# Kernel optimization log

Measured on AMD Instinct MI355X. Metric: run time of the kernel, lower is better.

The kernel has to match this reference:

```python
import jax, jax.numpy as jnp
import numpy as np

B, T, K, H = 256, 2048, 64, 256
NUM_PRED = 512


def setup_inputs() -> dict:
    key = jax.random.key(0)
    ks = jax.random.split(key, 13)
    s = 0.05
    G = 4 * H
    return {
        "input": jax.random.normal(ks[0], (B, T), jnp.float32),
        "conv_w": jax.random.normal(ks[1], (K,), jnp.float32) * s,
        "conv_b": jax.random.normal(ks[2], (K,), jnp.float32) * s,
        "W_ih0": jax.random.normal(ks[3], (G, K), jnp.float32) * s,
        "W_hh0": jax.random.normal(ks[4], (G, H), jnp.float32) * s,
        "b_ih0": jax.random.normal(ks[5], (G,), jnp.float32) * s,
        "b_hh0": jax.random.normal(ks[6], (G,), jnp.float32) * s,
        "W_ih1": jax.random.normal(ks[7], (G, H), jnp.float32) * s,
        "W_hh1": jax.random.normal(ks[8], (G, H), jnp.float32) * s,
        "b_ih1": jax.random.normal(ks[9], (G,), jnp.float32) * s,
        "b_hh1": jax.random.normal(ks[10], (G,), jnp.float32) * s,
        "lin_w": jax.random.normal(ks[11], (1, H), jnp.float32) * s,
        "lin_b": jax.random.normal(ks[12], (1,), jnp.float32) * s,
        "num_predictions": NUM_PRED,
    }


def _cell(x, h, c, Wi, Wh, bi, bh):
    # PyTorch LSTM cell: gate order i, f, g, o
    g = x @ Wi.T + h @ Wh.T + bi + bh
    i, f, gg, o = jnp.split(g, 4, axis=-1)
    i = jax.nn.sigmoid(i)
    f = jax.nn.sigmoid(f)
    gg = jnp.tanh(gg)
    o = jax.nn.sigmoid(o)
    c_new = f * c + i * gg
    h_new = o * jnp.tanh(c_new)
    return h_new, c_new


def reference(input, conv_w, conv_b, W_ih0, W_hh0, b_ih0, b_hh0,
              W_ih1, W_hh1, b_ih1, b_hh1, lin_w, lin_b, num_predictions):
    Bn, Tn = input.shape
    Kn = conv_w.shape[0]
    Hh = W_hh0.shape[1]

    # cnn: [B,1,T] -> Conv1d(1,K,1) -> [B,K,T] -> ReLU -> torch.reshape to (B,T,K)
    # NOTE: original uses reshape (not transpose); replicate faithfully.
    c_raw = jax.nn.relu(input[:, None, :] * conv_w[None, :, None] + conv_b[None, :, None])  # [B,K,T]
    c_out = c_raw.reshape(Bn, Tn, Kn)  # faithful reshape-as-in-source

    def step(carry, x):
        h0, c0, h1, c1 = carry
        h0, c0 = _cell(x, h0, c0, W_ih0, W_hh0, b_ih0, b_hh0)
        h1, c1 = _cell(h0, h1, c1, W_ih1, W_hh1, b_ih1, b_hh1)
        return (h0, c0, h1, c1), None

    z = jnp.zeros((Bn, Hh), input.dtype)
    carry, _ = jax.lax.scan(step, (z, z, z, z), jnp.swapaxes(c_out, 0, 1))  # scan over T
    pred0 = carry[2] @ lin_w.T + lin_b  # [B,1], output of last warmup step

    def ar_step(carry, _):
        h0, c0, h1, c1, last = carry
        x = jax.nn.relu(last[:, None] * conv_w[None, :] + conv_b[None, :])  # [B,K]
        h0, c0 = _cell(x, h0, c0, W_ih0, W_hh0, b_ih0, b_hh0)
        h1, c1 = _cell(h0, h1, c1, W_ih1, W_hh1, b_ih1, b_hh1)
        p = (h1 @ lin_w.T + lin_b)[:, 0]  # [B]
        return (h0, c0, h1, c1, p), p

    init = (*carry, pred0[:, 0])
    _, preds = jax.lax.scan(ar_step, init, None, length=num_predictions - 1)  # [P-1, B]
    return jnp.concatenate([pred0, preds.T], axis=1)  # [B, num_predictions]
```

## Files before the change

kernel.cpp:

```cpp
#include <hip/hip_runtime.h>
#include <hip/hip_bf16.h>
#include <cstdint>

#define TT 2048
#define NPRED 512
#define NSTEP (TT + NPRED)

typedef _Float16 f16;
typedef __attribute__((ext_vector_type(8))) _Float16 f16x8;
typedef __attribute__((ext_vector_type(4))) float f32x4;

#define WB0_OFF   0u
#define WB1_OFF   655360u
#define BIAS0_OFF 1703936u
#define BIAS1_OFF 1708032u
#define HX0_OFF   1712128u
#define HX1_OFF   2236416u
#define FLAG_OFF  2760704u
#define PACC_OFF  2768896u

static __device__ __forceinline__ float sigmoidf_(float x) {
    return 1.0f / (1.0f + __expf(-x));
}

static __device__ __forceinline__ float2 ld2a(const float* p) {
    unsigned long long v = __hip_atomic_load((const unsigned long long*)p,
                                             __ATOMIC_RELAXED, __HIP_MEMORY_SCOPE_AGENT);
    float2 r;
    r.x = __uint_as_float((unsigned)(v & 0xffffffffull));
    r.y = __uint_as_float((unsigned)(v >> 32));
    return r;
}
static __device__ __forceinline__ float ld1a(const float* p) {
    unsigned v = __hip_atomic_load((const unsigned*)p,
                                   __ATOMIC_RELAXED, __HIP_MEMORY_SCOPE_AGENT);
    return __uint_as_float(v);
}
static __device__ __forceinline__ void st1a(float* p, float v) {
    __hip_atomic_store((unsigned*)p, __float_as_uint(v),
                       __ATOMIC_RELAXED, __HIP_MEMORY_SCOPE_AGENT);
}

static __device__ __forceinline__ void split8(float2 q0, float2 q1, float2 q2, float2 q3,
                                              f16x8& hi, f16x8& lo) {
    float a[8] = {q0.x, q0.y, q1.x, q1.y, q2.x, q2.y, q3.x, q3.y};
    #pragma unroll
    for (int e = 0; e < 8; ++e) {
        f16 h = (f16)a[e];
        hi[e] = h;
        lo[e] = (f16)(a[e] - (float)h);
    }
}

#define N0_ELEM 327680
#define N1_ELEM 524288

__global__ __launch_bounds__(256) void prep_kernel(
    const float* __restrict__ W_ih0, const float* __restrict__ W_hh0,
    const float* __restrict__ b_ih0, const float* __restrict__ b_hh0,
    const float* __restrict__ W_ih1, const float* __restrict__ W_hh1,
    const float* __restrict__ b_ih1, const float* __restrict__ b_hh1,
    f16* __restrict__ WB0, f16* __restrict__ WB1,
    float* __restrict__ bias0P, float* __restrict__ bias1P,
    unsigned int* __restrict__ flags, float* __restrict__ p_part)
{
    int idx = blockIdx.x * 256 + threadIdx.x;
    if (idx < N0_ELEM) {
        int e = idx & 7, l = (idx >> 3) & 63;
        int rest = idx >> 9;
        int fr = rest % 10, sw = rest / 10;
        int w = sw & 3, slice = sw >> 2;
        int q = l & 3, jj = (l & 15) >> 2;
        int row = q * 256 + slice * 16 + 4 * w + jj;
        int k = fr * 32 + (l >> 4) * 8 + e;
        float v = (k < 64) ? W_ih0[row * 64 + k] : W_hh0[row * 256 + (k - 64)];
        WB0[idx] = (f16)v;
    } else if (idx < N0_ELEM + N1_ELEM) {
        int i2 = idx - N0_ELEM;
        int e = i2 & 7, l = (i2 >> 3) & 63;
        int rest = i2 >> 9;
        int fr = rest & 15, sw = rest >> 4;
        int w = sw & 3, slice = sw >> 2;
        int q = l & 3, jj = (l & 15) >> 2;
        int row = q * 256 + slice * 16 + 4 * w + jj;
        int k = fr * 32 + (l >> 4) * 8 + e;
        float v = (k < 256) ? W_ih1[row * 256 + k] : W_hh1[row * 256 + (k - 256)];
        WB1[i2] = (f16)v;
    } else if (idx < N0_ELEM + N1_ELEM + 1024) {
        int r = idx - (N0_ELEM + N1_ELEM);
        int j = r >> 2, q = r & 3;
        bias0P[r] = b_ih0[q * 256 + j] + b_hh0[q * 256 + j];
    } else if (idx < N0_ELEM + N1_ELEM + 2048) {
        int r = idx - (N0_ELEM + N1_ELEM + 1024);
        int j = r >> 2, q = r & 3;
        bias1P[r] = b_ih1[q * 256 + j] + b_hh1[q * 256 + j];
    } else if (idx < N0_ELEM + N1_ELEM + 2048 + 2048) {
        flags[idx - (N0_ELEM + N1_ELEM + 2048)] = 0u;
    } else if (idx < N0_ELEM + N1_ELEM + 2048 + 2048 + 8192) {
        p_part[idx - (N0_ELEM + N1_ELEM + 2048 + 2048)] = 0.f;
    }
}

__global__ __launch_bounds__(256) void fused_kernel(
    const float* __restrict__ input,
    const float* __restrict__ conv_w, const float* __restrict__ conv_b,
    const f16* __restrict__ WB0, const f16* __restrict__ WB1,
    const float* __restrict__ bias0P, const float* __restrict__ bias1P,
    const float* __restrict__ lin_w, const float* __restrict__ lin_b,
    float* hx0, float* hx1, unsigned int* flags, float* p_part,
    float* __restrict__ out)
{
    const int t = threadIdx.x;
    const int lane = t & 63, w = t >> 6;
    const int g = blockIdx.x & 15, slice = blockIdx.x >> 4;

    __shared__ __align__(16) f16 Ah[18 * 65 * 8];
    __shared__ __align__(16) f16 Al[18 * 65 * 8];
    __shared__ __align__(16) float gbuf0[16 * 68 + 4];
    __shared__ __align__(16) float gbuf1[16 * 68 + 4];
    __shared__ float cw_s[64], cb_s[64], lw_s[256];
    __shared__ float p_lds[16];

    f16x8 B0[10], B1[16];
    {
        const f16* p0 = WB0 + ((size_t)(slice * 4 + w) * 10 * 64 + lane) * 8;
        #pragma unroll
        for (int f = 0; f < 10; ++f) B0[f] = *(const f16x8*)(p0 + f * 512);
        const f16* p1 = WB1 + ((size_t)(slice * 4 + w) * 16 * 64 + lane) * 8;
        #pragma unroll
        for (int f = 0; f < 16; ++f) B1[f] = *(const f16x8*)(p1 + f * 512);
    }

    if (t < 64) { cw_s[t] = conv_w[t]; cb_s[t] = conv_b[t]; }
    lw_s[t] = lin_w[t];

    #pragma unroll
    for (int i = 0; i < 4; ++i) {
        int c = t + 256 * i;
        int d = ((2 + (c >> 6)) * 65 + (c & 63)) * 8;
        f16x8 z = {};
        *(f16x8*)(Ah + d) = z;
        *(f16x8*)(Al + d) = z;
    }

    const int ub = t >> 4, uj = t & 15;
    const int jg = slice * 16 + uj;
    const float4 bs0 = *(const float4*)(bias0P + 4 * jg);
    const float4 bs1 = *(const float4*)(bias1P + 4 * jg);
    float c0 = 0.f, c1 = 0.f;
    const float linb = lin_b[0];

    const int rb = t & 15;
    const int roct = t >> 4;
    const int bg0 = g * 16;

    unsigned int* fl0 = flags + (size_t)g * 64;
    unsigned int* cnp = flags + (size_t)(16 + g) * 64;

    __syncthreads();

    #pragma unroll 1
    for (int k = 0; k < TT; ++k) {
        if (k >= 1) {
            const float* src = hx0 + (size_t)((k - 1) & 1) * 65536 + (size_t)(bg0 + rb) * 256;
            #pragma unroll
            for (int it = 0; it < 2; ++it) {
                int oct = roct + 16 * it;
                float2 q0 = ld2a(src + oct * 8);
                float2 q1 = ld2a(src + oct * 8 + 2);
                float2 q2 = ld2a(src + oct * 8 + 4);
                float2 q3 = ld2a(src + oct * 8 + 6);
                f16x8 hv, lv;
                split8(q0, q1, q2, q3, hv, lv);
                int d = ((2 + (oct >> 2)) * 65 + (rb + 16 * (oct & 3))) * 8;
                *(f16x8*)(Ah + d) = hv;
                *(f16x8*)(Al + d) = lv;
            }
        }
        if (k >= 2) {
            const float* src = hx1 + (size_t)((k - 1) & 1) * 65536 + (size_t)(bg0 + rb) * 256;
            #pragma unroll
            for (int it = 0; it < 2; ++it) {
                int oct = roct + 16 * it;
                float2 q0 = ld2a(src + oct * 8);
                float2 q1 = ld2a(src + oct * 8 + 2);
                float2 q2 = ld2a(src + oct * 8 + 4);
                float2 q3 = ld2a(src + oct * 8 + 6);
                f16x8 hv, lv;
                split8(q0, q1, q2, q3, hv, lv);
                int d = ((10 + (oct >> 2)) * 65 + (rb + 16 * (oct & 3))) * 8;
                *(f16x8*)(Ah + d) = hv;
                *(f16x8*)(Al + d) = lv;
            }
        }
        if (roct < 8) {
            int k0 = roct * 8;
            const float* inprow = input + (size_t)(bg0 + rb) * TT + ((k & 31) << 6);
            float cwv = cw_s[k >> 5], cbv = cb_s[k >> 5];
            f16x8 hv, lv;
            #pragma unroll
            for (int e = 0; e < 8; ++e) {
                float xv = fmaxf(inprow[k0 + e] * cwv + cbv, 0.f);
                f16 h = (f16)xv;
                hv[e] = h;
                lv[e] = (f16)(xv - (float)h);
            }
            int d = ((roct >> 2) * 65 + (rb + 16 * (roct & 3))) * 8;
            *(f16x8*)(Ah + d) = hv;
            *(f16x8*)(Al + d) = lv;
        }
        __syncthreads();

        {
            f32x4 acc = {0.f, 0.f, 0.f, 0.f};
            #pragma unroll
            for (int f = 0; f < 10; ++f) {
                f16x8 ah = *(const f16x8*)(Ah + (f * 65 + lane) * 8);
                acc = __builtin_amdgcn_mfma_f32_16x16x32_f16(ah, B0[f], acc, 0, 0, 0);
                f16x8 al = *(const f16x8*)(Al + (f * 65 + lane) * 8);
                acc = __builtin_amdgcn_mfma_f32_16x16x32_f16(al, B0[f], acc, 0, 0, 0);
            }
            int rr = w * 16 + (lane & 15);
            int bb = (lane >> 4) * 4;
            #pragma unroll
            for (int qq = 0; qq < 4; ++qq) gbuf0[(bb + qq) * 68 + rr] = acc[qq];
        }
        if (k >= 1) {
            f32x4 acc = {0.f, 0.f, 0.f, 0.f};
            #pragma unroll
            for (int f = 0; f < 16; ++f) {
                f16x8 ah = *(const f16x8*)(Ah + ((2 + f) * 65 + lane) * 8);
                acc = __builtin_amdgcn_mfma_f32_16x16x32_f16(ah, B1[f], acc, 0, 0, 0);
                f16x8 al = *(const f16x8*)(Al + ((2 + f) * 65 + lane) * 8);
                acc = __builtin_amdgcn_mfma_f32_16x16x32_f16(al, B1[f], acc, 0, 0, 0);
            }
            int rr = w * 16 + (lane & 15);
            int bb = (lane >> 4) * 4;
            #pragma unroll
            for (int qq = 0; qq < 4; ++qq) gbuf1[(bb + qq) * 68 + rr] = acc[qq];
        }
        __syncthreads();

        {
            float4 gv = *(const float4*)(gbuf0 + ub * 68 + uj * 4);
            float gi = gv.x + bs0.x, gf = gv.y + bs0.y, gg = gv.z + bs0.z, go = gv.w + bs0.w;
            float cn = sigmoidf_(gf) * c0 + sigmoidf_(gi) * tanhf(gg);
            float hn = sigmoidf_(go) * tanhf(cn);
            c0 = cn;
            st1a(hx0 + (size_t)(k & 1) * 65536 + (size_t)(bg0 + ub) * 256 + jg, hn);
        }
        if (k >= 1) {
            float4 gv = *(const float4*)(gbuf1 + ub * 68 + uj * 4);
            float gi = gv.x + bs1.x, gf = gv.y + bs1.y, gg = gv.z + bs1.z, go = gv.w + bs1.w;
            float cn = sigmoidf_(gf) * c1 + sigmoidf_(gi) * tanhf(gg);
            float hn = sigmoidf_(go) * tanhf(cn);
            c1 = cn;
            st1a(hx1 + (size_t)(k & 1) * 65536 + (size_t)(bg0 + ub) * 256 + jg, hn);
        }
        __syncthreads();
        if (t == 0) {
            __hip_atomic_fetch_add(fl0, 1u, __ATOMIC_RELAXED, __HIP_MEMORY_SCOPE_AGENT);
            unsigned tgt = 16u * (unsigned)(k + 1);
            while (__hip_atomic_load(fl0, __ATOMIC_RELAXED, __HIP_MEMORY_SCOPE_AGENT) < tgt)
                __builtin_amdgcn_s_sleep(1);
        }
        __syncthreads();
    }

    #pragma unroll 1
    for (int k = TT; k < NSTEP; ++k) {
        {
            const float* s0 = hx0 + (size_t)((k - 1) & 1) * 65536 + (size_t)(bg0 + rb) * 256;
            const float* s1 = hx1 + (size_t)((k - 1) & 1) * 65536 + (size_t)(bg0 + rb) * 256;
            #pragma unroll
            for (int it = 0; it < 2; ++it) {
                int oct = roct + 16 * it;
                float2 q0 = ld2a(s0 + oct * 8);
                float2 q1 = ld2a(s0 + oct * 8 + 2);
                float2 q2 = ld2a(s0 + oct * 8 + 4);
                float2 q3 = ld2a(s0 + oct * 8 + 6);
                f16x8 hv, lv;
                split8(q0, q1, q2, q3, hv, lv);
                int d = ((2 + (oct >> 2)) * 65 + (rb + 16 * (oct & 3))) * 8;
                *(f16x8*)(Ah + d) = hv;
                *(f16x8*)(Al + d) = lv;
                float2 r0 = ld2a(s1 + oct * 8);
                float2 r1 = ld2a(s1 + oct * 8 + 2);
                float2 r2 = ld2a(s1 + oct * 8 + 4);
                float2 r3 = ld2a(s1 + oct * 8 + 6);
                split8(r0, r1, r2, r3, hv, lv);
                d = ((10 + (oct >> 2)) * 65 + (rb + 16 * (oct & 3))) * 8;
                *(f16x8*)(Ah + d) = hv;
                *(f16x8*)(Al + d) = lv;
            }
        }
        __syncthreads();

        {
            f32x4 acc = {0.f, 0.f, 0.f, 0.f};
            #pragma unroll
            for (int f = 0; f < 16; ++f) {
                f16x8 ah = *(const f16x8*)(Ah + ((2 + f) * 65 + lane) * 8);
                acc = __builtin_amdgcn_mfma_f32_16x16x32_f16(ah, B1[f], acc, 0, 0, 0);
                f16x8 al = *(const f16x8*)(Al + ((2 + f) * 65 + lane) * 8);
                acc = __builtin_amdgcn_mfma_f32_16x16x32_f16(al, B1[f], acc, 0, 0, 0);
            }
            int rr = w * 16 + (lane & 15);
            int bb = (lane >> 4) * 4;
            #pragma unroll
            for (int qq = 0; qq < 4; ++qq) gbuf1[(bb + qq) * 68 + rr] = acc[qq];
        }
        __syncthreads();

        {
            float4 gv = *(const float4*)(gbuf1 + ub * 68 + uj * 4);
            float gi = gv.x + bs1.x, gf = gv.y + bs1.y, gg = gv.z + bs1.z, go = gv.w + bs1.w;
            float cn = sigmoidf_(gf) * c1 + sigmoidf_(gi) * tanhf(gg);
            float hn = sigmoidf_(go) * tanhf(cn);
            c1 = cn;
            st1a(hx1 + (size_t)(k & 1) * 65536 + (size_t)(bg0 + ub) * 256 + jg, hn);
            float pp = hn * lw_s[jg];
            pp += __shfl_xor(pp, 1);
            pp += __shfl_xor(pp, 2);
            pp += __shfl_xor(pp, 4);
            pp += __shfl_xor(pp, 8);
            if (uj == 0)
                st1a(p_part + (size_t)(k & 1) * 4096 + (size_t)slice * 256 + (bg0 + ub), pp);
        }
        __syncthreads();
        if (t == 0) {
            __hip_atomic_fetch_add(cnp, 1u, __ATOMIC_RELAXED, __HIP_MEMORY_SCOPE_AGENT);
            unsigned tgt = 16u * (unsigned)(k - TT + 1);
            while (__hip_atomic_load(cnp, __ATOMIC_RELAXED, __HIP_MEMORY_SCOPE_AGENT) < tgt)
                __builtin_amdgcn_s_sleep(1);
        }
        __syncthreads();

        if (t < 16) {
            const float* pb = p_part + (size_t)(k & 1) * 4096;
            float ps = 0.f;
            #pragma unroll
            for (int sl = 0; sl < 16; ++sl) ps += ld1a(pb + sl * 256 + bg0 + t);
            float p = ps + linb;
            p_lds[t] = p;
            if (slice == 0) out[(size_t)(bg0 + t) * NPRED + (k - TT)] = p;
        }
        if (k == NSTEP - 1) break;
        __syncthreads();

        if (roct < 8) {
            int k0 = roct * 8;
            float p = p_lds[rb];
            f16x8 hv, lv;
            #pragma unroll
            for (int e = 0; e < 8; ++e) {
                float xv = fmaxf(p * cw_s[k0 + e] + cb_s[k0 + e], 0.f);
                f16 h = (f16)xv;
                hv[e] = h;
                lv[e] = (f16)(xv - (float)h);
            }
            int d = ((roct >> 2) * 65 + (rb + 16 * (roct & 3))) * 8;
            *(f16x8*)(Ah + d) = hv;
            *(f16x8*)(Al + d) = lv;
        }
        __syncthreads();

        {
            f32x4 acc = {0.f, 0.f, 0.f, 0.f};
            #pragma unroll
            for (int f = 0; f < 10; ++f) {
                f16x8 ah = *(const f16x8*)(Ah + (f * 65 + lane) * 8);
                acc = __builtin_amdgcn_mfma_f32_16x16x32_f16(ah, B0[f], acc, 0, 0, 0);
                f16x8 al = *(const f16x8*)(Al + (f * 65 + lane) * 8);
                acc = __builtin_amdgcn_mfma_f32_16x16x32_f16(al, B0[f], acc, 0, 0, 0);
            }
            int rr = w * 16 + (lane & 15);
            int bb = (lane >> 4) * 4;
            #pragma unroll
            for (int qq = 0; qq < 4; ++qq) gbuf0[(bb + qq) * 68 + rr] = acc[qq];
        }
        __syncthreads();
        {
            float4 gv = *(const float4*)(gbuf0 + ub * 68 + uj * 4);
            float gi = gv.x + bs0.x, gf = gv.y + bs0.y, gg = gv.z + bs0.z, go = gv.w + bs0.w;
            float cn = sigmoidf_(gf) * c0 + sigmoidf_(gi) * tanhf(gg);
            float hn = sigmoidf_(go) * tanhf(cn);
            c0 = cn;
            st1a(hx0 + (size_t)(k & 1) * 65536 + (size_t)(bg0 + ub) * 256 + jg, hn);
        }
        __syncthreads();
        if (t == 0) {
            __hip_atomic_fetch_add(fl0, 1u, __ATOMIC_RELAXED, __HIP_MEMORY_SCOPE_AGENT);
            unsigned tgt = 16u * (unsigned)(k + 1);
            while (__hip_atomic_load(fl0, __ATOMIC_RELAXED, __HIP_MEMORY_SCOPE_AGENT) < tgt)
                __builtin_amdgcn_s_sleep(1);
        }
        __syncthreads();
    }
}

extern "C" void kernel_launch(void* const* d_in, const int* in_sizes, int n_in,
                              void* d_out, int out_size, void* d_ws, size_t ws_size,
                              hipStream_t stream) {
    const float* input  = (const float*)d_in[0];
    const float* conv_w = (const float*)d_in[1];
    const float* conv_b = (const float*)d_in[2];
    const float* W_ih0  = (const float*)d_in[3];
    const float* W_hh0  = (const float*)d_in[4];
    const float* b_ih0  = (const float*)d_in[5];
    const float* b_hh0  = (const float*)d_in[6];
    const float* W_ih1  = (const float*)d_in[7];
    const float* W_hh1  = (const float*)d_in[8];
    const float* b_ih1  = (const float*)d_in[9];
    const float* b_hh1  = (const float*)d_in[10];
    const float* lin_w  = (const float*)d_in[11];
    const float* lin_b  = (const float*)d_in[12];
    float* out = (float*)d_out;

    uint8_t* ws = (uint8_t*)d_ws;
    f16* WB0 = (f16*)(ws + WB0_OFF);
    f16* WB1 = (f16*)(ws + WB1_OFF);
    float* bias0P = (float*)(ws + BIAS0_OFF);
    float* bias1P = (float*)(ws + BIAS1_OFF);
    float* hx0 = (float*)(ws + HX0_OFF);
    float* hx1 = (float*)(ws + HX1_OFF);
    unsigned int* flags = (unsigned int*)(ws + FLAG_OFF);
    float* p_part = (float*)(ws + PACC_OFF);

    prep_kernel<<<3376, 256, 0, stream>>>(W_ih0, W_hh0, b_ih0, b_hh0,
                                          W_ih1, W_hh1, b_ih1, b_hh1,
                                          WB0, WB1, bias0P, bias1P, flags, p_part);

    fused_kernel<<<256, 256, 0, stream>>>(input, conv_w, conv_b,
                                          WB0, WB1, bias0P, bias1P,
                                          lin_w, lin_b, hx0, hx1, flags, p_part, out);
}
```

Measured before the change: 11.40 ms.

## Store hidden states as fp16 and drop hi/lo split MFMA passes

Hidden states exchanged between blocks through global memory are now stored as packed fp16 instead of fp32. Adjacent lanes pair their values with a shuffle so each store writes one 32-bit word. The split-fp16 (hi+lo) emulation of fp32 activations is removed, which halves the MFMA count and removes the Al LDS buffer and the split conversion work. This cuts global traffic and compute on the latency-bound recurrent critical path, at the cost of fp16 rounding of activations accumulating over 2560 recurrent steps, which may hurt accuracy.

```diff
diff --git a/kernel.cpp b/kernel.cpp
--- a/kernel.cpp
+++ b/kernel.cpp
@@ -15,21 +15,18 @@
 #define BIAS0_OFF 1703936u
 #define BIAS1_OFF 1708032u
 #define HX0_OFF   1712128u
-#define HX1_OFF   2236416u
-#define FLAG_OFF  2760704u
-#define PACC_OFF  2768896u
+#define HX1_OFF   1974272u
+#define FLAG_OFF  2236416u
+#define PACC_OFF  2244608u
 
 static __device__ __forceinline__ float sigmoidf_(float x) {
     return 1.0f / (1.0f + __expf(-x));
 }
 
-static __device__ __forceinline__ float2 ld2a(const float* p) {
+static __device__ __forceinline__ uint2 ld8u(const unsigned short* p) {
     unsigned long long v = __hip_atomic_load((const unsigned long long*)p,
                                              __ATOMIC_RELAXED, __HIP_MEMORY_SCOPE_AGENT);
-    float2 r;
-    r.x = __uint_as_float((unsigned)(v & 0xffffffffull));
-    r.y = __uint_as_float((unsigned)(v >> 32));
-    return r;
+    uint2 r; r.x = (unsigned)v; r.y = (unsigned)(v >> 32); return r;
 }
 static __device__ __forceinline__ float ld1a(const float* p) {
     unsigned v = __hip_atomic_load((const unsigned*)p,
@@ -40,16 +37,13 @@
     __hip_atomic_store((unsigned*)p, __float_as_uint(v),
                        __ATOMIC_RELAXED, __HIP_MEMORY_SCOPE_AGENT);
 }
-
-static __device__ __forceinline__ void split8(float2 q0, float2 q1, float2 q2, float2 q3,
-                                              f16x8& hi, f16x8& lo) {
-    float a[8] = {q0.x, q0.y, q1.x, q1.y, q2.x, q2.y, q3.x, q3.y};
-    #pragma unroll
-    for (int e = 0; e < 8; ++e) {
-        f16 h = (f16)a[e];
-        hi[e] = h;
-        lo[e] = (f16)(a[e] - (float)h);
-    }
+static __device__ __forceinline__ void st4a(unsigned* p, unsigned v) {
+    __hip_atomic_store(p, v, __ATOMIC_RELAXED, __HIP_MEMORY_SCOPE_AGENT);
+}
+static __device__ __forceinline__ unsigned short f16bits(float x) {
+    union { f16 h; unsigned short u; } cv;
+    cv.h = (f16)x;
+    return cv.u;
 }
 
 #define N0_ELEM 327680
@@ -107,7 +101,8 @@
     const f16* __restrict__ WB0, const f16* __restrict__ WB1,
     const float* __restrict__ bias0P, const float* __restrict__ bias1P,
     const float* __restrict__ lin_w, const float* __restrict__ lin_b,
-    float* hx0, float* hx1, unsigned int* flags, float* p_part,
+    unsigned short* hx0, unsigned short* hx1,
+    unsigned int* flags, float* p_part,
     float* __restrict__ out)
 {
     const int t = threadIdx.x;
@@ -115,7 +110,6 @@
     const int g = blockIdx.x & 15, slice = blockIdx.x >> 4;
 
     __shared__ __align__(16) f16 Ah[18 * 65 * 8];
-    __shared__ __align__(16) f16 Al[18 * 65 * 8];
     __shared__ __align__(16) float gbuf0[16 * 68 + 4];
     __shared__ __align__(16) float gbuf1[16 * 68 + 4];
     __shared__ float cw_s[64], cb_s[64], lw_s[256];
@@ -140,7 +134,6 @@
         int d = ((2 + (c >> 6)) * 65 + (c & 63)) * 8;
         f16x8 z = {};
         *(f16x8*)(Ah + d) = z;
-        *(f16x8*)(Al + d) = z;
     }
 
     const int ub = t >> 4, uj = t & 15;
@@ -151,7 +144,7 @@
     const float linb = lin_b[0];
 
     const int rb = t & 15;
-    const int roct = t >> 4;
+    const int rest = t >> 4;
     const int bg0 = g * 16;
 
     unsigned int* fl0 = flags + (size_t)g * 64;
@@ -162,52 +155,38 @@
     #pragma unroll 1
     for (int k = 0; k < TT; ++k) {
         if (k >= 1) {
-            const float* src = hx0 + (size_t)((k - 1) & 1) * 65536 + (size_t)(bg0 + rb) * 256;
+            const unsigned short* s0 = hx0 + (size_t)((k - 1) & 1) * 65536 + (size_t)(bg0 + rb) * 256;
             #pragma unroll
             for (int it = 0; it < 2; ++it) {
-                int oct = roct + 16 * it;
-                float2 q0 = ld2a(src + oct * 8);
-                float2 q1 = ld2a(src + oct * 8 + 2);
-                float2 q2 = ld2a(src + oct * 8 + 4);
-                float2 q3 = ld2a(src + oct * 8 + 6);
-                f16x8 hv, lv;
-                split8(q0, q1, q2, q3, hv, lv);
+                int oct = rest + 16 * it;
+                uint2 a = ld8u(s0 + oct * 8);
+                uint2 b = ld8u(s0 + oct * 8 + 4);
                 int d = ((2 + (oct >> 2)) * 65 + (rb + 16 * (oct & 3))) * 8;
-                *(f16x8*)(Ah + d) = hv;
-                *(f16x8*)(Al + d) = lv;
+                *(uint4*)(Ah + d) = make_uint4(a.x, a.y, b.x, b.y);
             }
         }
         if (k >= 2) {
-            const float* src = hx1 + (size_t)((k - 1) & 1) * 65536 + (size_t)(bg0 + rb) * 256;
+            const unsigned short* s1 = hx1 + (size_t)((k - 1) & 1) * 65536 + (size_t)(bg0 + rb) * 256;
             #pragma unroll
             for (int it = 0; it < 2; ++it) {
-                int oct = roct + 16 * it;
-                float2 q0 = ld2a(src + oct * 8);
-                float2 q1 = ld2a(src + oct * 8 + 2);
-                float2 q2 = ld2a(src + oct * 8 + 4);
-                float2 q3 = ld2a(src + oct * 8 + 6);
-                f16x8 hv, lv;
-                split8(q0, q1, q2, q3, hv, lv);
+                int oct = rest + 16 * it;
+                uint2 a = ld8u(s1 + oct * 8);
+                uint2 b = ld8u(s1 + oct * 8 + 4);
                 int d = ((10 + (oct >> 2)) * 65 + (rb + 16 * (oct & 3))) * 8;
-                *(f16x8*)(Ah + d) = hv;
-                *(f16x8*)(Al + d) = lv;
-            }
-        }
-        if (roct < 8) {
-            int k0 = roct * 8;
-            const float* inprow = input + (size_t)(bg0 + rb) * TT + ((k & 31) << 6);
+                *(uint4*)(Ah + d) = make_uint4(a.x, a.y, b.x, b.y);
+            }
+        }
+        if (t < 128) {
+            int rb2 = t & 15, xoct = t >> 4;
+            int k0 = xoct * 8;
+            const float* inprow = input + (size_t)(bg0 + rb2) * TT + ((k & 31) << 6);
             float cwv = cw_s[k >> 5], cbv = cb_s[k >> 5];
-            f16x8 hv, lv;
-            #pragma unroll
-            for (int e = 0; e < 8; ++e) {
-                float xv = fmaxf(inprow[k0 + e] * cwv + cbv, 0.f);
-                f16 h = (f16)xv;
-                hv[e] = h;
-                lv[e] = (f16)(xv - (float)h);
-            }
-            int d = ((roct >> 2) * 65 + (rb + 16 * (roct & 3))) * 8;
+            f16x8 hv;
+            #pragma unroll
+            for (int e = 0; e < 8; ++e)
+                hv[e] = (f16)fmaxf(inprow[k0 + e] * cwv + cbv, 0.f);
+            int d = ((xoct >> 2) * 65 + (rb2 + 16 * (xoct & 3))) * 8;
             *(f16x8*)(Ah + d) = hv;
-            *(f16x8*)(Al + d) = lv;
         }
         __syncthreads();
 
@@ -215,10 +194,8 @@
             f32x4 acc = {0.f, 0.f, 0.f, 0.f};
             #pragma unroll
             for (int f = 0; f < 10; ++f) {
-                f16x8 ah = *(const f16x8*)(Ah + (f * 65 + lane) * 8);
-                acc = __builtin_amdgcn_mfma_f32_16x16x32_f16(ah, B0[f], acc, 0, 0, 0);
-                f16x8 al = *(const f16x8*)(Al + (f * 65 + lane) * 8);
-                acc = __builtin_amdgcn_mfma_f32_16x16x32_f16(al, B0[f], acc, 0, 0, 0);
+                f16x8 a = *(const f16x8*)(Ah + (f * 65 + lane) * 8);
+                acc = __builtin_amdgcn_mfma_f32_16x16x32_f16(a, B0[f], acc, 0, 0, 0);
             }
             int rr = w * 16 + (lane & 15);
             int bb = (lane >> 4) * 4;
@@ -229,10 +206,8 @@
             f32x4 acc = {0.f, 0.f, 0.f, 0.f};
             #pragma unroll
             for (int f = 0; f < 16; ++f) {
-                f16x8 ah = *(const f16x8*)(Ah + ((2 + f) * 65 + lane) * 8);
-                acc = __builtin_amdgcn_mfma_f32_16x16x32_f16(ah, B1[f], acc, 0, 0, 0);
-                f16x8 al = *(const f16x8*)(Al + ((2 + f) * 65 + lane) * 8);
-                acc = __builtin_amdgcn_mfma_f32_16x16x32_f16(al, B1[f], acc, 0, 0, 0);
+                f16x8 a = *(const f16x8*)(Ah + ((2 + f) * 65 + lane) * 8);
+                acc = __builtin_amdgcn_mfma_f32_16x16x32_f16(a, B1[f], acc, 0, 0, 0);
             }
             int rr = w * 16 + (lane & 15);
             int bb = (lane >> 4) * 4;
@@ -247,7 +222,12 @@
             float cn = sigmoidf_(gf) * c0 + sigmoidf_(gi) * tanhf(gg);
             float hn = sigmoidf_(go) * tanhf(cn);
             c0 = cn;
-            st1a(hx0 + (size_t)(k & 1) * 65536 + (size_t)(bg0 + ub) * 256 + jg, hn);
+            unsigned short hb = f16bits(hn);
+            int oth = __shfl_xor((int)hb, 1);
+            if (!(uj & 1)) {
+                unsigned word = (unsigned)hb | ((unsigned)(oth & 0xffff) << 16);
+                st4a((unsigned*)(hx0 + (size_t)(k & 1) * 65536 + (size_t)(bg0 + ub) * 256 + jg), word);
+            }
         }
         if (k >= 1) {
             float4 gv = *(const float4*)(gbuf1 + ub * 68 + uj * 4);
@@ -255,7 +235,12 @@
             float cn = sigmoidf_(gf) * c1 + sigmoidf_(gi) * tanhf(gg);
             float hn = sigmoidf_(go) * tanhf(cn);
             c1 = cn;
-            st1a(hx1 + (size_t)(k & 1) * 65536 + (size_t)(bg0 + ub) * 256 + jg, hn);
+            unsigned short hb = f16bits(hn);
+            int oth = __shfl_xor((int)hb, 1);
+            if (!(uj & 1)) {
+                unsigned word = (unsigned)hb | ((unsigned)(oth & 0xffff) << 16);
+                st4a((unsigned*)(hx1 + (size_t)(k & 1) * 65536 + (size_t)(bg0 + ub) * 256 + jg), word);
+            }
         }
         __syncthreads();
         if (t == 0) {
@@ -270,28 +255,19 @@
     #pragma unroll 1
     for (int k = TT; k < NSTEP; ++k) {
         {
-            const float* s0 = hx0 + (size_t)((k - 1) & 1) * 65536 + (size_t)(bg0 + rb) * 256;
-            const float* s1 = hx1 + (size_t)((k - 1) & 1) * 65536 + (size_t)(bg0 + rb) * 256;
+            const unsigned short* s0 = hx0 + (size_t)((k - 1) & 1) * 65536 + (size_t)(bg0 + rb) * 256;
+            const unsigned short* s1 = hx1 + (size_t)((k - 1) & 1) * 65536 + (size_t)(bg0 + rb) * 256;
             #pragma unroll
             for (int it = 0; it < 2; ++it) {
-                int oct = roct + 16 * it;
-                float2 q0 = ld2a(s0 + oct * 8);
-                float2 q1 = ld2a(s0 + oct * 8 + 2);
-                float2 q2 = ld2a(s0 + oct * 8 + 4);
-                float2 q3 = ld2a(s0 + oct * 8 + 6);
-                f16x8 hv, lv;
-                split8(q0, q1, q2, q3, hv, lv);
+                int oct = rest + 16 * it;
+                uint2 a0 = ld8u(s0 + oct * 8);
+                uint2 b0 = ld8u(s0 + oct * 8 + 4);
                 int d = ((2 + (oct >> 2)) * 65 + (rb + 16 * (oct & 3))) * 8;
-                *(f16x8*)(Ah + d) = hv;
-                *(f16x8*)(Al + d) = lv;
-                float2 r0 = ld2a(s1 + oct * 8);
-                float2 r1 = ld2a(s1 + oct * 8 + 2);
-                float2 r2 = ld2a(s1 + oct * 8 + 4);
-                float2 r3 = ld2a(s1 + oct * 8 + 6);
-                split8(r0, r1, r2, r3, hv, lv);
+                *(uint4*)(Ah + d) = make_uint4(a0.x, a0.y, b0.x, b0.y);
+                uint2 a1 = ld8u(s1 + oct * 8);
+                uint2 b1 = ld8u(s1 + oct * 8 + 4);
                 d = ((10 + (oct >> 2)) * 65 + (rb + 16 * (oct & 3))) * 8;
-                *(f16x8*)(Ah + d) = hv;
-                *(f16x8*)(Al + d) = lv;
+                *(uint4*)(Ah + d) = make_uint4(a1.x, a1.y, b1.x, b1.y);
             }
         }
         __syncthreads();
@@ -300,10 +276,8 @@
             f32x4 acc = {0.f, 0.f, 0.f, 0.f};
             #pragma unroll
             for (int f = 0; f < 16; ++f) {
-                f16x8 ah = *(const f16x8*)(Ah + ((2 + f) * 65 + lane) * 8);
-                acc = __builtin_amdgcn_mfma_f32_16x16x32_f16(ah, B1[f], acc, 0, 0, 0);
-                f16x8 al = *(const f16x8*)(Al + ((2 + f) * 65 + lane) * 8);
-                acc = __builtin_amdgcn_mfma_f32_16x16x32_f16(al, B1[f], acc, 0, 0, 0);
+                f16x8 a = *(const f16x8*)(Ah + ((2 + f) * 65 + lane) * 8);
+                acc = __builtin_amdgcn_mfma_f32_16x16x32_f16(a, B1[f], acc, 0, 0, 0);
             }
             int rr = w * 16 + (lane & 15);
             int bb = (lane >> 4) * 4;
@@ -318,7 +292,12 @@
             float cn = sigmoidf_(gf) * c1 + sigmoidf_(gi) * tanhf(gg);
             float hn = sigmoidf_(go) * tanhf(cn);
             c1 = cn;
-            st1a(hx1 + (size_t)(k & 1) * 65536 + (size_t)(bg0 + ub) * 256 + jg, hn);
+            unsigned short hb = f16bits(hn);
+            int oth = __shfl_xor((int)hb, 1);
+            if (!(uj & 1)) {
+                unsigned word = (unsigned)hb | ((unsigned)(oth & 0xffff) << 16);
+                st4a((unsigned*)(hx1 + (size_t)(k & 1) * 65536 + (size_t)(bg0 + ub) * 256 + jg), word);
+            }
             float pp = hn * lw_s[jg];
             pp += __shfl_xor(pp, 1);
             pp += __shfl_xor(pp, 2);
@@ -348,20 +327,16 @@
         if (k == NSTEP - 1) break;
         __syncthreads();
 
-        if (roct < 8) {
-            int k0 = roct * 8;
-            float p = p_lds[rb];
-            f16x8 hv, lv;
-            #pragma unroll
-            for (int e = 0; e < 8; ++e) {
-                float xv = fmaxf(p * cw_s[k0 + e] + cb_s[k0 + e], 0.f);
-                f16 h = (f16)xv;
-                hv[e] = h;
-                lv[e] = (f16)(xv - (float)h);
-            }
-            int d = ((roct >> 2) * 65 + (rb + 16 * (roct & 3))) * 8;
+        if (t < 128) {
+            int rb2 = t & 15, xoct = t >> 4;
+            int k0 = xoct * 8;
+            float p = p_lds[rb2];
+            f16x8 hv;
+            #pragma unroll
+            for (int e = 0; e < 8; ++e)
+                hv[e] = (f16)fmaxf(p * cw_s[k0 + e] + cb_s[k0 + e], 0.f);
+            int d = ((xoct >> 2) * 65 + (rb2 + 16 * (xoct & 3))) * 8;
             *(f16x8*)(Ah + d) = hv;
-            *(f16x8*)(Al + d) = lv;
         }
         __syncthreads();
 
@@ -369,10 +344,8 @@
             f32x4 acc = {0.f, 0.f, 0.f, 0.f};
             #pragma unroll
             for (int f = 0; f < 10; ++f) {
-                f16x8 ah = *(const f16x8*)(Ah + (f * 65 + lane) * 8);
-                acc = __builtin_amdgcn_mfma_f32_16x16x32_f16(ah, B0[f], acc, 0, 0, 0);
-                f16x8 al = *(const f16x8*)(Al + (f * 65 + lane) * 8);
-                acc = __builtin_amdgcn_mfma_f32_16x16x32_f16(al, B0[f], acc, 0, 0, 0);
+                f16x8 a = *(const f16x8*)(Ah + (f * 65 + lane) * 8);
+                acc = __builtin_amdgcn_mfma_f32_16x16x32_f16(a, B0[f], acc, 0, 0, 0);
             }
             int rr = w * 16 + (lane & 15);
             int bb = (lane >> 4) * 4;
@@ -386,7 +359,12 @@
             float cn = sigmoidf_(gf) * c0 + sigmoidf_(gi) * tanhf(gg);
             float hn = sigmoidf_(go) * tanhf(cn);
             c0 = cn;
-            st1a(hx0 + (size_t)(k & 1) * 65536 + (size_t)(bg0 + ub) * 256 + jg, hn);
+            unsigned short hb = f16bits(hn);
+            int oth = __shfl_xor((int)hb, 1);
+            if (!(uj & 1)) {
+                unsigned word = (unsigned)hb | ((unsigned)(oth & 0xffff) << 16);
+                st4a((unsigned*)(hx0 + (size_t)(k & 1) * 65536 + (size_t)(bg0 + ub) * 256 + jg), word);
+            }
         }
         __syncthreads();
         if (t == 0) {
@@ -422,8 +400,8 @@
     f16* WB1 = (f16*)(ws + WB1_OFF);
     float* bias0P = (float*)(ws + BIAS0_OFF);
     float* bias1P = (float*)(ws + BIAS1_OFF);
-    float* hx0 = (float*)(ws + HX0_OFF);
-    float* hx1 = (float*)(ws + HX1_OFF);
+    unsigned short* hx0 = (unsigned short*)(ws + HX0_OFF);
+    unsigned short* hx1 = (unsigned short*)(ws + HX1_OFF);
     unsigned int* flags = (unsigned int*)(ws + FLAG_OFF);
     float* p_part = (float*)(ws + PACC_OFF);
 
```

New measurement: 9.296 ms, median of 2. 18.5% less time.
